# Kernel optimization log

Measured on AMD Instinct MI355X. Metric: run time of the kernel, lower is better.

Reference implementation:

```python
import jax, jax.numpy as jnp
import numpy as np
import math

HIDDEN = 1024
NUM_HEADS = 16
HEAD_DIM = HIDDEN // NUM_HEADS
B, S = 4, 1024


def setup_inputs() -> dict:
    key = jax.random.key(0)
    ks = jax.random.split(key, 16)
    sd = 1.0 / math.sqrt(HIDDEN)
    inp = {
        "x": jax.random.normal(ks[0], (B, S, HIDDEN), jnp.float32),
        "spikes": jax.random.uniform(ks[1], (B, S, HIDDEN), jnp.float32),
        "membrane_potential": jax.random.normal(ks[2], (B, S, HIDDEN), jnp.float32),
        "Wq": jax.random.normal(ks[3], (HIDDEN, HIDDEN), jnp.float32) * sd,
        "bq": jnp.zeros((HIDDEN,), jnp.float32),
        "Wk": jax.random.normal(ks[4], (HIDDEN, HIDDEN), jnp.float32) * sd,
        "bk": jnp.zeros((HIDDEN,), jnp.float32),
        "Wv": jax.random.normal(ks[5], (HIDDEN, HIDDEN), jnp.float32) * sd,
        "bv": jnp.zeros((HIDDEN,), jnp.float32),
        "Wo": jax.random.normal(ks[6], (HIDDEN, HIDDEN), jnp.float32) * sd,
        "bo": jnp.zeros((HIDDEN,), jnp.float32),
        "tau_decay": jnp.ones((NUM_HEADS,), jnp.float32) * 10.0,
        "Wg": jax.random.normal(ks[7], (HIDDEN, 2 * HIDDEN), jnp.float32) * sd,
        "bg": jnp.zeros((HIDDEN,), jnp.float32),
    }
    return inp


def _heads(t):  # [B,S,H] -> [B,nH,S,hd]
    Bv, Sv, _ = t.shape
    return t.reshape(Bv, Sv, NUM_HEADS, HEAD_DIM).transpose(0, 2, 1, 3)


def reference(x, spikes, membrane_potential, Wq, bq, Wk, bk, Wv, bv, Wo, bo, tau_decay, Wg, bg):
    scale = 1.0 / math.sqrt(HEAD_DIM)
    q = _heads(x @ Wq.T + bq)
    k = _heads(x @ Wk.T + bk)
    v = _heads(x @ Wv.T + bv)

    # raw scores [B,nH,S,S]
    scores = jnp.einsum('bhqd,bhkd->bhqk', q, k) * scale

    # per-head exponential temporal decay mask [nH,S,S]
    times = jnp.arange(S, dtype=jnp.float32)
    tdiff = jnp.abs(times[:, None] - times[None, :])  # [S,S]
    tmask = jnp.exp(-tdiff[None] / tau_decay[:, None, None])
    scores = scores * tmask[None]

    # spike correlation term
    sm = _heads(spikes)
    spike_attn = jnp.einsum('bhqd,bhkd->bhqk', sm, sm) * scale
    scores = scores * (1.0 + spike_attn)

    # membrane gating of V
    v = v * jax.nn.sigmoid(_heads(membrane_potential))

    probs = jax.nn.softmax(scores, axis=-1)
    context = jnp.einsum('bhqk,bhkd->bhqd', probs, v)
    context = context.transpose(0, 2, 1, 3).reshape(B, S, HIDDEN)

    # dendritic gate
    gate_in = jnp.concatenate([context, membrane_potential], axis=-1)
    gate = jax.nn.sigmoid(gate_in @ Wg.T + bg)
    context = context * gate

    return context @ Wo.T + bo
```

## Files before the change

kernel.cpp:

```cpp
#include <hip/hip_runtime.h>
#include <math.h>
#include <stdint.h>

namespace {

typedef __attribute__((ext_vector_type(8))) short s8v;
typedef __attribute__((ext_vector_type(4))) float f4v;
typedef unsigned short u16;

__device__ __forceinline__ float fexp2(float x) {
  return __builtin_amdgcn_exp2f(x);
}

__device__ __forceinline__ u16 f2bf(float f) {
  union { float f; uint32_t u; } v; v.f = f;
  uint32_t r = v.u + 0x7fffu + ((v.u >> 16) & 1u);
  return (u16)(r >> 16);
}
__device__ __forceinline__ float bf2f(u16 h) {
  union { uint32_t u; float f; } v; v.u = ((uint32_t)h) << 16;
  return v.f;
}
__device__ __forceinline__ uint32_t pk2r(float a, float b) {
  return (uint32_t)f2bf(a) | ((uint32_t)f2bf(b) << 16);
}
__device__ __forceinline__ uint32_t pk2(float a, float b) {
  union { float f; uint32_t u; } x, y; x.f = a; y.f = b;
  return ((x.u + 0x8000u) >> 16) | ((y.u + 0x8000u) & 0xffff0000u);
}
__device__ __forceinline__ float sigmoidf_(float x) { return 1.0f / (1.0f + __expf(-x)); }

__device__ __forceinline__ void gload16(const u16* g, u16* l) {
  __builtin_amdgcn_global_load_lds(
      (const __attribute__((address_space(1))) void*)g,
      (__attribute__((address_space(3))) void*)l, 16, 0, 0);
}

struct CvtJob { const float* src; u16* dst; };
struct CvtArgs { CvtJob j[18]; float* vz; };

__global__ __launch_bounds__(256) void cvt_kernel(CvtArgs a) {
  if (blockIdx.y == 0 && blockIdx.x < 4) {
    float4 z; z.x = 0.f; z.y = 0.f; z.z = 0.f; z.w = 0.f;
    ((float4*)a.vz)[blockIdx.x * 256 + threadIdx.x] = z;
  }
  const CvtJob jb = a.j[blockIdx.y];
  const int i = blockIdx.x * 256 + threadIdx.x;
  const float4 v = ((const float4*)jb.src)[i];
  uint2 pk;
  pk.x = pk2r(v.x, v.y);
  pk.y = pk2r(v.z, v.w);
  ((uint2*)jb.dst)[i] = pk;
}

__global__ __launch_bounds__(384, 3) void qkv_gemm(
    const u16* __restrict__ xb,
    const u16* __restrict__ Wqb, const u16* __restrict__ Wkb, const u16* __restrict__ Wvb,
    const float* __restrict__ bq, const float* __restrict__ bk, const float* __restrict__ bv,
    const u16* __restrict__ memb,
    u16* __restrict__ Qb, u16* __restrict__ Kb, u16* __restrict__ Vt,
    float* __restrict__ Vtot) {
  __shared__ __align__(16) u16 as_[2][4096];
  __shared__ __align__(16) u16 bs_[2][6144];
  const int t = threadIdx.x;
  const int nb = blockIdx.x, mb = blockIdx.y;
  const int m0 = mb * 128, n0 = nb * 64;
  const int l = t & 63, w = t >> 6;
  const int mat = w >> 1;
  const int wm = w & 1;
  const int lr = l & 15, lq = l >> 4;
  const int rh = lr >> 1;
  const int rb4 = (lr & 1) << 2;
  const int bmat = mat * 2048;

  const f4v fz = {0.f, 0.f, 0.f, 0.f};
  f4v acc[4][4];
#pragma unroll
  for (int i = 0; i < 4; ++i)
#pragma unroll
    for (int j = 0; j < 4; ++j) acc[i][j] = fz;

  const int sc0a = (t & 7) ^ ((t >> 3) & 7);
  const int sgrowa = (((t & 255) >> 3) << 1) + (sc0a >> 2);
  const int sgka = (sc0a & 3) << 3;
  const u16* ga0 = xb + (size_t)(m0 + sgrowa) * 1024 + sgka;
  const u16* ga1 = xb + (size_t)(m0 + 64 + sgrowa) * 1024 + sgka;
  const int tq1 = t & 255;
  const int tq2 = (t < 128) ? (t + 128) : (t - 128);
  const u16* wb1 = (t < 256) ? Wqb : Wkb;
  const u16* wb2 = (t < 128) ? Wkb : Wvb;
  const int sc01 = (tq1 & 7) ^ ((tq1 >> 3) & 7);
  const int sc02 = (tq2 & 7) ^ ((tq2 >> 3) & 7);
  const u16* gb1 = wb1 + (size_t)(n0 + ((tq1 >> 3) << 1) + (sc01 >> 2)) * 1024 +
                   ((sc01 & 3) << 3);
  const u16* gb2 = wb2 + (size_t)(n0 + ((tq2 >> 3) << 1) + (sc02 >> 2)) * 1024 +
                   ((sc02 & 3) << 3);
  const int mb1 = ((t < 256) ? 0 : 2048) + tq1 * 8;
  const int mb2 = ((t < 128) ? 2048 : 4096) + tq2 * 8;

#define QKV_STAGE(c)                                                           \
  {                                                                            \
    const int ko_ = (c) * 32;                                                  \
    const int bb_ = (c) & 1;                                                   \
    if (t < 256) {                                                             \
      gload16(ga0 + ko_, &as_[bb_][(t & 255) * 8]);                            \
      gload16(ga1 + ko_, &as_[bb_][2048 + (t & 255) * 8]);                     \
    }                                                                          \
    gload16(gb1 + ko_, &bs_[bb_][mb1]);                                        \
    gload16(gb2 + ko_, &bs_[bb_][mb2]);                                        \
  }

  QKV_STAGE(0); QKV_STAGE(1);
  if (w < 4) {
    asm volatile("s_waitcnt vmcnt(4)" ::: "memory");
  } else {
    asm volatile("s_waitcnt vmcnt(2)" ::: "memory");
  }
  __builtin_amdgcn_s_barrier();

  const int co = ((rb4 + lq) ^ rh) * 8;
  for (int c = 0; c < 32; ++c) {
    const int cb = c & 1;
    s8v af[4], bf[4];
#pragma unroll
    for (int mi = 0; mi < 4; ++mi)
      af[mi] = *(const s8v*)(&as_[cb][(wm * 32 + mi * 8 + rh) * 64 + co]);
#pragma unroll
    for (int ni = 0; ni < 4; ++ni)
      bf[ni] = *(const s8v*)(&bs_[cb][bmat + (ni * 8 + rh) * 64 + co]);
    asm volatile("s_waitcnt lgkmcnt(0)" ::: "memory");
    __builtin_amdgcn_sched_barrier(0);
    __builtin_amdgcn_s_barrier();
    if (c + 2 < 32) QKV_STAGE(c + 2);
    __builtin_amdgcn_s_setprio(1);
    if (mat < 2) {
#pragma unroll
      for (int mi = 0; mi < 4; ++mi)
#pragma unroll
        for (int ni = 0; ni < 4; ++ni)
          acc[mi][ni] = __builtin_amdgcn_mfma_f32_16x16x32_bf16(
              bf[ni], af[mi], acc[mi][ni], 0, 0, 0);
    } else {
#pragma unroll
      for (int mi = 0; mi < 4; ++mi)
#pragma unroll
        for (int ni = 0; ni < 4; ++ni)
          acc[mi][ni] = __builtin_amdgcn_mfma_f32_16x16x32_bf16(
              af[mi], bf[ni], acc[mi][ni], 0, 0, 0);
    }
    __builtin_amdgcn_s_setprio(0);
    if (c + 2 < 32) {
      if (w < 4) {
        asm volatile("s_waitcnt vmcnt(4)" ::: "memory");
      } else {
        asm volatile("s_waitcnt vmcnt(2)" ::: "memory");
      }
    } else if (c == 30) {
      asm volatile("s_waitcnt vmcnt(0)" ::: "memory");
    }
    if (c < 31) __builtin_amdgcn_s_barrier();
  }
#undef QKV_STAGE
  __builtin_amdgcn_sched_barrier(0);

  if (mat < 2) {
    u16* dst = (mat == 0) ? Qb : Kb;
    const float* bias = (mat == 0) ? bq : bk;
#pragma unroll
    for (int mi = 0; mi < 4; ++mi)
#pragma unroll
      for (int ni = 0; ni < 4; ++ni) {
        const int m = m0 + wm * 64 + mi * 16 + lr;
        const int nb4 = n0 + ni * 16 + lq * 4;
        const float4 b4 = *(const float4*)&bias[nb4];
        uint2 pk;
        pk.x = pk2r(acc[mi][ni][0] + b4.x, acc[mi][ni][1] + b4.y);
        pk.y = pk2r(acc[mi][ni][2] + b4.z, acc[mi][ni][3] + b4.w);
        *(uint2*)(dst + (size_t)m * 1024 + nb4) = pk;
      }
  } else {
    const int b = m0 >> 10;
    float vpart[4] = {0.f, 0.f, 0.f, 0.f};
#pragma unroll
    for (int mi = 0; mi < 4; ++mi)
#pragma unroll
      for (int ni = 0; ni < 4; ++ni) {
        const int mrow = m0 + wm * 64 + mi * 16 + lq * 4;
        const int ncol = n0 + ni * 16 + lr;
        const int h = ncol >> 6, d = ncol & 63;
        const float bi = bv[ncol];
        float tv[4];
#pragma unroll
        for (int r = 0; r < 4; ++r)
          tv[r] = (acc[mi][ni][r] + bi) *
                  sigmoidf_(bf2f(memb[(size_t)(mrow + r) * 1024 + ncol]));
        vpart[ni] += (tv[0] + tv[1]) + (tv[2] + tv[3]);
        const int s = mrow & 1023;
        uint2 pk;
        pk.x = pk2r(tv[0], tv[1]);
        pk.y = pk2r(tv[2], tv[3]);
        *(uint2*)(Vt + ((size_t)((b * 16 + h) * 64 + d)) * 1024 + s) = pk;
      }
#pragma unroll
    for (int ni = 0; ni < 4; ++ni) {
      const int ncol = n0 + ni * 16 + lr;
      atomicAdd(&Vtot[(size_t)(b * 16 + (ncol >> 6)) * 64 + (ncol & 63)], vpart[ni]);
    }
  }
}

template <int MODE>
__global__ __launch_bounds__(512, 2) void gemm64(
    const u16* __restrict__ Ab, const u16* __restrict__ A2b,
    const u16* __restrict__ W, const float* __restrict__ bias,
    u16* __restrict__ outb, float* __restrict__ outf, int K) {
  __shared__ __align__(16) u16 as_[4][4096], bs_[4][4096];
  const int t = threadIdx.x;
  const int m0 = blockIdx.y * 128, n0 = blockIdx.x * 128;
  const int l = t & 63, w = t >> 6;
  const int wm = w >> 2, wn = w & 3;
  const int lr = l & 15, lq = l >> 4;
  const int rh = lr >> 1, rb4 = (lr & 1) << 2;
  const f4v fz = {0.f, 0.f, 0.f, 0.f};
  f4v acc[4][2];
#pragma unroll
  for (int i = 0; i < 4; ++i)
#pragma unroll
    for (int j = 0; j < 2; ++j) acc[i][j] = fz;

  const int tt = t & 255, uu = t >> 8;
  const int sc0 = (tt & 7) ^ ((tt >> 3) & 7);
  const int sgrow = ((tt >> 3) << 1) + (sc0 >> 2);
  const int sgk = (sc0 & 3) << 3;
  const u16* ga1 = Ab + (size_t)(m0 + uu * 64 + sgrow) * 1024 + sgk;
  const u16* ga2 = (MODE == 1)
      ? (A2b + (size_t)(m0 + uu * 64 + sgrow) * 1024 + sgk) : ga1;
  const u16* gw = W + (size_t)(n0 + uu * 64 + sgrow) * K + sgk;
  const int lofs = uu * 2048 + tt * 8;
  const int nc = K >> 5;

#define G_STAGE_A(c)                                                           \
  {                                                                            \
    const int ko_ = (c) * 32;                                                  \
    if (MODE == 1 && ko_ >= 1024) gload16(ga2 + (ko_ - 1024), &as_[(c) & 3][lofs]); \
    else gload16(ga1 + ko_, &as_[(c) & 3][lofs]);                              \
  }
#define G_STAGE_W(c) gload16(gw + (c) * 32, &bs_[(c) & 3][lofs])

  G_STAGE_A(0); G_STAGE_W(0);
  G_STAGE_A(1); G_STAGE_W(1);
  G_STAGE_A(2); G_STAGE_W(2);
  asm volatile("s_waitcnt vmcnt(4)" ::: "memory");
  __builtin_amdgcn_s_barrier();

  const int co = ((rb4 + lq) ^ rh) * 8;
  for (int c = 0; c < nc; ++c) {
    const int cb = c & 3;
    s8v af[4], bf[2];
#pragma unroll
    for (int mi = 0; mi < 4; ++mi)
      af[mi] = *(const s8v*)(&as_[cb][(wm * 32 + mi * 8 + rh) * 64 + co]);
#pragma unroll
    for (int ni = 0; ni < 2; ++ni)
      bf[ni] = *(const s8v*)(&bs_[cb][(wn * 16 + ni * 8 + rh) * 64 + co]);
    if (c + 3 < nc) { G_STAGE_A(c + 3); G_STAGE_W(c + 3); }
    __builtin_amdgcn_s_barrier();
    asm volatile("s_waitcnt lgkmcnt(0)" ::: "memory");
    __builtin_amdgcn_sched_barrier(0);
    __builtin_amdgcn_s_setprio(1);
#pragma unroll
    for (int mi = 0; mi < 4; ++mi)
#pragma unroll
      for (int ni = 0; ni < 2; ++ni)
        acc[mi][ni] = __builtin_amdgcn_mfma_f32_16x16x32_bf16(
            bf[ni], af[mi], acc[mi][ni], 0, 0, 0);
    __builtin_amdgcn_s_setprio(0);
    if (c + 3 < nc) {
      asm volatile("s_waitcnt vmcnt(4)" ::: "memory");
    } else if (c + 3 == nc) {
      asm volatile("s_waitcnt vmcnt(2)" ::: "memory");
    } else if (c + 2 == nc) {
      asm volatile("s_waitcnt vmcnt(0)" ::: "memory");
    }
    if (c + 1 < nc) __builtin_amdgcn_s_barrier();
  }
#undef G_STAGE_A
#undef G_STAGE_W
  __builtin_amdgcn_sched_barrier(0);

#pragma unroll
  for (int mi = 0; mi < 4; ++mi)
#pragma unroll
    for (int ni = 0; ni < 2; ++ni) {
      const int m = m0 + wm * 64 + mi * 16 + lr;
      const int nb4 = n0 + wn * 32 + ni * 16 + lq * 4;
      const float4 b4 = *(const float4*)&bias[nb4];
      if (MODE == 0) {
        float4 o;
        o.x = acc[mi][ni][0] + b4.x; o.y = acc[mi][ni][1] + b4.y;
        o.z = acc[mi][ni][2] + b4.z; o.w = acc[mi][ni][3] + b4.w;
        *(float4*)(outf + (size_t)m * 1024 + nb4) = o;
      } else {
        const uint2 a2 = *(const uint2*)(Ab + (size_t)m * 1024 + nb4);
        float cx[4] = {bf2f((u16)(a2.x & 0xffff)), bf2f((u16)(a2.x >> 16)),
                       bf2f((u16)(a2.y & 0xffff)), bf2f((u16)(a2.y >> 16))};
        float g[4];
        g[0] = cx[0] * sigmoidf_(acc[mi][ni][0] + b4.x);
        g[1] = cx[1] * sigmoidf_(acc[mi][ni][1] + b4.y);
        g[2] = cx[2] * sigmoidf_(acc[mi][ni][2] + b4.z);
        g[3] = cx[3] * sigmoidf_(acc[mi][ni][3] + b4.w);
        uint2 pk;
        pk.x = pk2r(g[0], g[1]);
        pk.y = pk2r(g[2], g[3]);
        *(uint2*)(outb + (size_t)m * 1024 + nb4) = pk;
      }
    }
}

__global__ __launch_bounds__(256) void attn_mfma(
    const u16* __restrict__ Qb, const u16* __restrict__ Kb,
    const u16* __restrict__ SPb, const u16* __restrict__ Vt,
    const float* __restrict__ tau, const float* __restrict__ Vtot,
    u16* __restrict__ CTXb) {
  __shared__ u16 kbuf[4096], skbuf[4096], vbuf[4096];
  __shared__ u16 pbuf[4][16 * 64];
  const int t = threadIdx.x, l = t & 63, w = t >> 6;
  const int lr = l & 15, lq = l >> 4;
  const int p = blockIdx.x;
  const int g = (p & 7) + 8 * (p >> 7);
  const int qt = (p >> 3) & 15;
  const int h = g & 15, b = g >> 4;

  const float tv_ = tau[h];
  const float c2 = 1.44269504088896f / tv_;
  const float K0 = 0.125f * 1.44269504088896f;
  int rad = (int)ceilf(tv_ * 0.171875f);
  if (rad > 15) rad = 15;
  const int jlo = (qt - rad < 0) ? 0 : qt - rad;
  const int jhi = (qt + rad > 15) ? 15 : qt + rad;
  const int farCnt = 16 - (jhi - jlo + 1);

  float cN[4], cNi[4], cR[4], cRi[4];
#pragma unroll
  for (int i = 0; i < 4; ++i) {
    cN[i]  = fexp2(c2 * (float)(i * 16));
    cNi[i] = fexp2(-c2 * (float)(i * 16));
    cR[i]  = fexp2(c2 * (float)(lq * 4 + i));
    cRi[i] = fexp2(-c2 * (float)(lq * 4 + i));
  }

  s8v qf[2], sf[2];
  {
    const size_t base = ((size_t)(b * 1024 + qt * 64 + w * 16 + lr)) * 1024 + h * 64 + lq * 8;
    qf[0] = *(const s8v*)(Qb + base);
    qf[1] = *(const s8v*)(Qb + base + 32);
    sf[0] = *(const s8v*)(SPb + base);
    sf[1] = *(const s8v*)(SPb + base + 32);
  }
  const s8v ones = {0x3F80, 0x3F80, 0x3F80, 0x3F80, 0x3F80, 0x3F80, 0x3F80, 0x3F80};

  const f4v fz = {0.f, 0.f, 0.f, 0.f};
  f4v oacc[4], vs[4];
  float lacc[4];
#pragma unroll
  for (int i = 0; i < 4; ++i) { oacc[i] = fz; vs[i] = fz; lacc[i] = 0.f; }

  const int iqw = qt * 64 + w * 16;
  const int srow = t >> 3;
  const int csw = ((t & 7) ^ (srow & 7)) * 8;
  const int rx = lr & 7;
  u16* pw = pbuf[w];

  for (int jc = jlo; jc <= jhi; ++jc) {
    const int j0 = jc * 64;
    __syncthreads();
    {
      const size_t kg = ((size_t)(b * 1024 + j0 + srow)) * 1024 + h * 64 + csw;
      gload16(Kb + kg, kbuf + t * 8);
      gload16(Kb + kg + 32 * 1024, kbuf + 2048 + t * 8);
      gload16(SPb + kg, skbuf + t * 8);
      gload16(SPb + kg + 32 * 1024, skbuf + 2048 + t * 8);
      const size_t vg = ((size_t)((b * 16 + h) * 64 + srow)) * 1024 + j0 + csw;
      gload16(Vt + vg, vbuf + t * 8);
      gload16(Vt + vg + 32 * 1024, vbuf + 2048 + t * 8);
    }
    __syncthreads();

    f4v sa[4], ssa[4];
#pragma unroll
    for (int ni = 0; ni < 4; ++ni) { sa[ni] = fz; ssa[ni] = fz; }
#pragma unroll
    for (int ks = 0; ks < 2; ++ks) {
#pragma unroll
      for (int ni = 0; ni < 4; ++ni) {
        const int off = (ni * 16 + lr) * 64 + (((ks * 4 + lq) ^ rx) * 8);
        const s8v kf = *(const s8v*)(kbuf + off);
        sa[ni] = __builtin_amdgcn_mfma_f32_16x16x32_bf16(kf, qf[ks], sa[ni], 0, 0, 0);
        const s8v skf = *(const s8v*)(skbuf + off);
        ssa[ni] = __builtin_amdgcn_mfma_f32_16x16x32_bf16(skf, sf[ks], ssa[ni], 0, 0, 0);
      }
    }

    const int D0 = iqw - j0;
    float pv[4][4];
    if (jc < qt) {
      const float EA = K0 * fexp2(-c2 * (float)(D0 + lr));
#pragma unroll
      for (int ni = 0; ni < 4; ++ni)
#pragma unroll
        for (int r = 0; r < 4; ++r) {
          const float t1 = fmaf(ssa[ni][r], 0.125f, 1.0f);
          const float e = fexp2(sa[ni][r] * cN[ni] * cR[r] * EA * t1);
          pv[ni][r] = e;
          lacc[ni] += e;
        }
    } else if (jc > qt) {
      const float EAi = K0 * fexp2(c2 * (float)(D0 + lr));
#pragma unroll
      for (int ni = 0; ni < 4; ++ni)
#pragma unroll
        for (int r = 0; r < 4; ++r) {
          const float t1 = fmaf(ssa[ni][r], 0.125f, 1.0f);
          const float e = fexp2(sa[ni][r] * cNi[ni] * cRi[r] * EAi * t1);
          pv[ni][r] = e;
          lacc[ni] += e;
        }
    } else {
      const float EA  = K0 * fexp2(-c2 * (float)(D0 + lr));
      const float EAi = K0 * fexp2(c2 * (float)(D0 + lr));
#pragma unroll
      for (int ni = 0; ni < 4; ++ni)
#pragma unroll
        for (int r = 0; r < 4; ++r) {
          const int jloc = ni * 16 + lq * 4 + r;
          const float fb = cN[ni] * cR[r] * EA;
          const float fa = cNi[ni] * cRi[r] * EAi;
          const float f = (D0 + lr >= jloc) ? fb : fa;
          const float t1 = fmaf(ssa[ni][r], 0.125f, 1.0f);
          const float e = fexp2(sa[ni][r] * f * t1);
          pv[ni][r] = e;
          lacc[ni] += e;
        }
    }

#pragma unroll
    for (int ni = 0; ni < 4; ++ni) {
      const int phys = (ni * 2 + (lq >> 1)) ^ rx;
      uint2 p2;
      p2.x = pk2(pv[ni][0], pv[ni][1]);
      p2.y = pk2(pv[ni][2], pv[ni][3]);
      *(uint2*)(pw + lr * 64 + phys * 8 + (lq & 1) * 4) = p2;
    }

#pragma unroll
    for (int ks = 0; ks < 2; ++ks) {
      const s8v pf = *(const s8v*)(pw + lr * 64 + (((ks * 4 + lq) ^ rx) * 8));
#pragma unroll
      for (int nd = 0; nd < 4; ++nd) {
        const int off = (nd * 16 + lr) * 64 + (((ks * 4 + lq) ^ rx) * 8);
        const s8v vf = *(const s8v*)(vbuf + off);
        oacc[nd] = __builtin_amdgcn_mfma_f32_16x16x32_bf16(vf, pf, oacc[nd], 0, 0, 0);
        vs[nd] = __builtin_amdgcn_mfma_f32_16x16x32_bf16(vf, ones, vs[nd], 0, 0, 0);
      }
    }
  }

  float ls = (lacc[0] + lacc[1]) + (lacc[2] + lacc[3]);
  ls += __shfl_xor(ls, 16);
  ls += __shfl_xor(ls, 32);
  ls += 64.0f * (float)farCnt;
  const float inv = 1.0f / ls;
  const float* vt0 = Vtot + (size_t)(b * 16 + h) * 64;
  const size_t orow = ((size_t)(b * 1024 + qt * 64 + w * 16 + lr)) * 1024 + h * 64;
#pragma unroll
  for (int nd = 0; nd < 4; ++nd) {
    const float4 vt4 = *(const float4*)(vt0 + nd * 16 + lq * 4);
    float o0 = (oacc[nd][0] + vt4.x - vs[nd][0]) * inv;
    float o1 = (oacc[nd][1] + vt4.y - vs[nd][1]) * inv;
    float o2 = (oacc[nd][2] + vt4.z - vs[nd][2]) * inv;
    float o3 = (oacc[nd][3] + vt4.w - vs[nd][3]) * inv;
    uint2 o;
    o.x = pk2r(o0, o1);
    o.y = pk2r(o2, o3);
    *(uint2*)(CTXb + orow + nd * 16 + lq * 4) = o;
  }
}

}

extern "C" void kernel_launch(void* const* d_in, const int* in_sizes, int n_in,
                              void* d_out, int out_size, void* d_ws, size_t ws_size,
                              hipStream_t stream) {
  const float* x      = (const float*)d_in[0];
  const float* spikes = (const float*)d_in[1];
  const float* mem    = (const float*)d_in[2];
  const float* Wq     = (const float*)d_in[3];
  const float* bq     = (const float*)d_in[4];
  const float* Wk     = (const float*)d_in[5];
  const float* bk     = (const float*)d_in[6];
  const float* Wv     = (const float*)d_in[7];
  const float* bv     = (const float*)d_in[8];
  const float* Wo     = (const float*)d_in[9];
  const float* bo     = (const float*)d_in[10];
  const float* tau    = (const float*)d_in[11];
  const float* Wg     = (const float*)d_in[12];
  const float* bg     = (const float*)d_in[13];
  float* out = (float*)d_out;

  uint8_t* w8 = (uint8_t*)d_ws;
  u16* spb  = (u16*)(w8);
  u16* xb   = (u16*)(w8 + (8u << 20));
  u16* Wqb  = (u16*)(w8 + (16u << 20));
  u16* Wkb  = (u16*)(w8 + (18u << 20));
  u16* Wvb  = (u16*)(w8 + (20u << 20));
  u16* Wob  = (u16*)(w8 + (22u << 20));
  u16* Wgb  = (u16*)(w8 + (24u << 20));
  u16* Qb   = (u16*)(w8 + (28u << 20));
  u16* Kb   = (u16*)(w8 + (36u << 20));
  u16* Vt   = (u16*)(w8 + (44u << 20));
  u16* CTXb = (u16*)(w8 + (52u << 20));
  float* Vtot = (float*)(w8 + (60u << 20));
  u16* memb = (u16*)d_out;
  u16* gctx = xb;

  constexpr size_t QE = 262144 * 4;
  CvtArgs ca;
  for (int q = 0; q < 4; ++q) ca.j[q]     = {x + q * QE,      xb + q * QE};
  for (int q = 0; q < 4; ++q) ca.j[4 + q] = {spikes + q * QE, spb + q * QE};
  for (int q = 0; q < 4; ++q) ca.j[8 + q] = {mem + q * QE,    memb + q * QE};
  ca.j[12] = {Wq, Wqb};
  ca.j[13] = {Wk, Wkb};
  ca.j[14] = {Wv, Wvb};
  ca.j[15] = {Wo, Wob};
  ca.j[16] = {Wg, Wgb};
  ca.j[17] = {Wg + QE, Wgb + QE};
  ca.vz = Vtot;
  cvt_kernel<<<dim3(1024, 18), 256, 0, stream>>>(ca);

  qkv_gemm<<<dim3(16, 32), 384, 0, stream>>>(xb, Wqb, Wkb, Wvb, bq, bk, bv, memb,
                                             Qb, Kb, Vt, Vtot);
  attn_mfma<<<dim3(1024), 256, 0, stream>>>(Qb, Kb, spb, Vt, tau, Vtot, CTXb);
  gemm64<1><<<dim3(8, 32), 512, 0, stream>>>(CTXb, memb, Wgb, bg, gctx, nullptr, 2048);
  gemm64<0><<<dim3(8, 32), 512, 0, stream>>>(gctx, nullptr, Wob, bo, nullptr, out, 1024);
}
```

Measured before the change: 250.3 us.

## Retile output GEMMs to 128x64 blocks of 128 threads with double buffering

The gate and output-projection GEMMs now use 128-thread blocks with 128x64 output tiles. Each wave computes a 64x64 sub-tile (4x4 MFMA accumulators) instead of 32x32, and the grid grows from 256 to 512 blocks. The shared-memory pipeline drops from four stages to two, which shrinks LDS per block and lets more blocks be resident. In exchange, each wave does more register-heavy work per step, and the shallower prefetch exposes more memory latency per block.

```diff
diff --git a/kernel.cpp b/kernel.cpp
--- a/kernel.cpp
+++ b/kernel.cpp
@@ -210,90 +210,89 @@
 }
 
 template <int MODE>
-__global__ __launch_bounds__(512, 2) void gemm64(
+__global__ __launch_bounds__(128, 4) void gemm64(
     const u16* __restrict__ Ab, const u16* __restrict__ A2b,
     const u16* __restrict__ W, const float* __restrict__ bias,
     u16* __restrict__ outb, float* __restrict__ outf, int K) {
-  __shared__ __align__(16) u16 as_[4][4096], bs_[4][4096];
+  __shared__ __align__(16) u16 as_[2][4096];
+  __shared__ __align__(16) u16 bs_[2][2048];
   const int t = threadIdx.x;
-  const int m0 = blockIdx.y * 128, n0 = blockIdx.x * 128;
+  const int m0 = blockIdx.y * 128, n0 = blockIdx.x * 64;
   const int l = t & 63, w = t >> 6;
-  const int wm = w >> 2, wn = w & 3;
   const int lr = l & 15, lq = l >> 4;
   const int rh = lr >> 1, rb4 = (lr & 1) << 2;
   const f4v fz = {0.f, 0.f, 0.f, 0.f};
-  f4v acc[4][2];
+  f4v acc[4][4];
 #pragma unroll
   for (int i = 0; i < 4; ++i)
 #pragma unroll
-    for (int j = 0; j < 2; ++j) acc[i][j] = fz;
-
-  const int tt = t & 255, uu = t >> 8;
-  const int sc0 = (tt & 7) ^ ((tt >> 3) & 7);
-  const int sgrow = ((tt >> 3) << 1) + (sc0 >> 2);
-  const int sgk = (sc0 & 3) << 3;
-  const u16* ga1 = Ab + (size_t)(m0 + uu * 64 + sgrow) * 1024 + sgk;
-  const u16* ga2 = (MODE == 1)
-      ? (A2b + (size_t)(m0 + uu * 64 + sgrow) * 1024 + sgk) : ga1;
-  const u16* gw = W + (size_t)(n0 + uu * 64 + sgrow) * K + sgk;
-  const int lofs = uu * 2048 + tt * 8;
+    for (int j = 0; j < 4; ++j) acc[i][j] = fz;
+
+  const int sc1 = (t & 7) ^ ((t >> 3) & 7);
+  const int gr1 = ((t >> 3) << 1) + (sc1 >> 2);
+  const int gk1 = (sc1 & 3) << 3;
+  const u16* gA = Ab + (size_t)(m0 + gr1) * 1024 + gk1;
+  const u16* gA2 = (MODE == 1) ? (A2b + (size_t)(m0 + gr1) * 1024 + gk1) : gA;
+  const u16* gW = W + (size_t)(n0 + gr1) * K + gk1;
+  const size_t wstep = (size_t)32 * K;
   const int nc = K >> 5;
 
-#define G_STAGE_A(c)                                                           \
+#define G_STAGE(c)                                                             \
   {                                                                            \
-    const int ko_ = (c) * 32;                                                  \
-    if (MODE == 1 && ko_ >= 1024) gload16(ga2 + (ko_ - 1024), &as_[(c) & 3][lofs]); \
-    else gload16(ga1 + ko_, &as_[(c) & 3][lofs]);                              \
-  }
-#define G_STAGE_W(c) gload16(gw + (c) * 32, &bs_[(c) & 3][lofs])
-
-  G_STAGE_A(0); G_STAGE_W(0);
-  G_STAGE_A(1); G_STAGE_W(1);
-  G_STAGE_A(2); G_STAGE_W(2);
-  asm volatile("s_waitcnt vmcnt(4)" ::: "memory");
+    const int c_ = (c);                                                        \
+    const u16* ab_ = (MODE == 1 && c_ >= 32) ? gA2 : gA;                       \
+    const int ko_ = ((MODE == 1 && c_ >= 32) ? (c_ - 32) : c_) * 32;           \
+    const int bb_ = c_ & 1;                                                    \
+    gload16(ab_ + ko_,             &as_[bb_][t * 8]);                          \
+    gload16(ab_ + 32 * 1024 + ko_, &as_[bb_][(t + 128) * 8]);                  \
+    gload16(ab_ + 64 * 1024 + ko_, &as_[bb_][2048 + t * 8]);                   \
+    gload16(ab_ + 96 * 1024 + ko_, &as_[bb_][2048 + (t + 128) * 8]);           \
+    gload16(gW + c_ * 32,          &bs_[bb_][t * 8]);                          \
+    gload16(gW + wstep + c_ * 32,  &bs_[bb_][(t + 128) * 8]);                  \
+  }
+
+  G_STAGE(0); G_STAGE(1);
+  asm volatile("s_waitcnt vmcnt(6)" ::: "memory");
   __builtin_amdgcn_s_barrier();
 
   const int co = ((rb4 + lq) ^ rh) * 8;
   for (int c = 0; c < nc; ++c) {
-    const int cb = c & 3;
-    s8v af[4], bf[2];
+    const int cb = c & 1;
+    s8v af[4], bf[4];
 #pragma unroll
     for (int mi = 0; mi < 4; ++mi)
-      af[mi] = *(const s8v*)(&as_[cb][(wm * 32 + mi * 8 + rh) * 64 + co]);
-#pragma unroll
-    for (int ni = 0; ni < 2; ++ni)
-      bf[ni] = *(const s8v*)(&bs_[cb][(wn * 16 + ni * 8 + rh) * 64 + co]);
-    if (c + 3 < nc) { G_STAGE_A(c + 3); G_STAGE_W(c + 3); }
-    __builtin_amdgcn_s_barrier();
+      af[mi] = *(const s8v*)(&as_[cb][w * 2048 + (mi * 8 + rh) * 64 + co]);
+#pragma unroll
+    for (int ni = 0; ni < 4; ++ni)
+      bf[ni] = *(const s8v*)(&bs_[cb][(ni * 8 + rh) * 64 + co]);
     asm volatile("s_waitcnt lgkmcnt(0)" ::: "memory");
     __builtin_amdgcn_sched_barrier(0);
+    __builtin_amdgcn_s_barrier();
+    if (c + 2 < nc) G_STAGE(c + 2);
     __builtin_amdgcn_s_setprio(1);
 #pragma unroll
     for (int mi = 0; mi < 4; ++mi)
 #pragma unroll
-      for (int ni = 0; ni < 2; ++ni)
+      for (int ni = 0; ni < 4; ++ni)
         acc[mi][ni] = __builtin_amdgcn_mfma_f32_16x16x32_bf16(
             bf[ni], af[mi], acc[mi][ni], 0, 0, 0);
     __builtin_amdgcn_s_setprio(0);
-    if (c + 3 < nc) {
-      asm volatile("s_waitcnt vmcnt(4)" ::: "memory");
-    } else if (c + 3 == nc) {
-      asm volatile("s_waitcnt vmcnt(2)" ::: "memory");
+    if (c + 2 < nc) {
+      asm volatile("s_waitcnt vmcnt(6)" ::: "memory");
     } else if (c + 2 == nc) {
       asm volatile("s_waitcnt vmcnt(0)" ::: "memory");
     }
     if (c + 1 < nc) __builtin_amdgcn_s_barrier();
   }
-#undef G_STAGE_A
-#undef G_STAGE_W
+#undef G_STAGE
   __builtin_amdgcn_sched_barrier(0);
 
 #pragma unroll
   for (int mi = 0; mi < 4; ++mi)
 #pragma unroll
-    for (int ni = 0; ni < 2; ++ni) {
-      const int m = m0 + wm * 64 + mi * 16 + lr;
-      const int nb4 = n0 + wn * 32 + ni * 16 + lq * 4;
+    for (int ni = 0; ni < 4; ++ni) {
+      const int m = m0 + w * 64 + mi * 16 + lr;
+      const int nb4 = n0 + ni * 16 + lq * 4;
       const float4 b4 = *(const float4*)&bias[nb4];
       if (MODE == 0) {
         float4 o;
@@ -540,6 +539,6 @@
   qkv_gemm<<<dim3(16, 32), 384, 0, stream>>>(xb, Wqb, Wkb, Wvb, bq, bk, bv, memb,
                                              Qb, Kb, Vt, Vtot);
   attn_mfma<<<dim3(1024), 256, 0, stream>>>(Qb, Kb, spb, Vt, tau, Vtot, CTXb);
-  gemm64<1><<<dim3(8, 32), 512, 0, stream>>>(CTXb, memb, Wgb, bg, gctx, nullptr, 2048);
-  gemm64<0><<<dim3(8, 32), 512, 0, stream>>>(gctx, nullptr, Wob, bo, nullptr, out, 1024);
-}
+  gemm64<1><<<dim3(16, 32), 128, 0, stream>>>(CTXb, memb, Wgb, bg, gctx, nullptr, 2048);
+  gemm64<0><<<dim3(16, 32), 128, 0, stream>>>(gctx, nullptr, Wob, bo, nullptr, out, 1024);
+}
```

New measurement: 260.3 us. 1.04x slower.
